# Performance work log

Measured on AMD Instinct MI355X. Metric: run time of the kernel, lower is better.

## Reference

```python
import jax, jax.numpy as jnp
import numpy as np

N = 25000        # nodes
E = 400000       # edges (avg 16 neighbors)
C1 = 8           # output_size (scalar channels into TP)
COUT = 16        # channels_out
LMAX = 2
NB = 8           # number_of_basis
RMAX = 5.0       # max_radius
EMB = 16         # atom embedding dim
NATOM = 10
WNUM = (LMAX + 1) * C1 * COUT                 # per-edge TP weights (parity-shared, k0 paths)
TOTAL_DIM = 2 * COUT * (1 + 3 + 9)            # both parities x ranks 0..2 -> 416


def setup_inputs() -> dict:
    key = jax.random.key(0)
    ks = jax.random.split(key, 12)
    rn = lambda i, shape, s=1.0: jax.random.normal(ks[i], shape, jnp.float32) * s
    pos = rn(0, (N, 3)) * 3.0
    A = jax.random.randint(ks[1], (N,), 0, NATOM)
    batch = jnp.zeros((N,), jnp.int32)                       # single graph
    edge_src = jax.random.randint(ks[2], (E,), 0, N)
    # avoid self-edges (zero-length vectors)
    edge_dst = (edge_src + jax.random.randint(ks[3], (E,), 1, N)) % N
    edge_shifts = jnp.zeros((E, 3), jnp.float32)
    cell = jnp.eye(3, dtype=jnp.float32)[None] * 10.0        # [1,3,3]
    emb_table = rn(4, (NATOM, EMB))
    atom_w1 = rn(5, (EMB, 64), EMB ** -0.5)
    atom_b1 = jnp.zeros((64,), jnp.float32)
    atom_w2 = rn(6, (64, C1), 64 ** -0.5)
    atom_b2 = jnp.zeros((C1,), jnp.float32)
    fc_w1 = rn(7, (NB, 64), NB ** -0.5)
    fc_b1 = jnp.zeros((64,), jnp.float32)
    fc_w2 = rn(8, (64, 64), 64 ** -0.5)
    fc_b2 = jnp.zeros((64,), jnp.float32)
    fc_w3 = rn(9, (64, WNUM), 64 ** -0.5)
    fc_b3 = jnp.zeros((WNUM,), jnp.float32)
    return dict(pos=pos, A=A, batch=batch, edge_src=edge_src, edge_dst=edge_dst,
                edge_shifts=edge_shifts, cell=cell, emb_table=emb_table,
                atom_w1=atom_w1, atom_b1=atom_b1, atom_w2=atom_w2, atom_b2=atom_b2,
                fc_w1=fc_w1, fc_b1=fc_b1, fc_w2=fc_w2, fc_b2=fc_b2, fc_w3=fc_w3, fc_b3=fc_b3)


def reference(pos, A, batch, edge_src, edge_dst, edge_shifts, cell, emb_table,
              atom_w1, atom_b1, atom_w2, atom_b2,
              fc_w1, fc_b1, fc_w2, fc_b2, fc_w3, fc_b3):
    num_edges = edge_src.shape[0]
    num_nodes = pos.shape[0]
    # edge geometry (PBC shift)
    edge_cells = cell[batch[edge_src]]                                   # [E,3,3]
    shift_vecs = jnp.einsum('ni,nij->nj', edge_shifts, edge_cells)
    edge_vec = pos[edge_dst] - pos[edge_src] + shift_vecs                # [E,3]
    edge_length = jnp.sqrt(jnp.sum(edge_vec * edge_vec, axis=1) + 1e-12)
    # per-node scalar features -> gathered to edges
    Ai = jax.nn.silu(emb_table[A] @ atom_w1 + atom_b1) @ atom_w2 + atom_b2  # [N,C1]
    Ai_e = Ai[edge_src]                                                    # [E,C1]
    # edge_rank_powers (normalized): rank-0 scalar 1, rank-1 u, rank-2 u\otimes u
    u = edge_vec / edge_length[:, None]
    # radial basis: e3nn soft_one_hot_linspace (gaussian, cutoff) * sqrt(NB)
    values = jnp.linspace(0.0, RMAX, NB + 2)[1:-1]
    step = RMAX / (NB + 1)
    diff = (edge_length[:, None] - values) / step
    emb = (jnp.exp(-diff * diff) / 1.12) * (NB ** 0.5)                     # [E,NB]
    # radial MLP -> per-edge TP weights
    h = jax.nn.silu(emb @ fc_w1 + fc_b1)
    h = jax.nn.silu(h @ fc_w2 + fc_b2)
    w = (h @ fc_w3 + fc_b3).reshape(num_edges, LMAX + 1, C1, COUT)
    # sparse cartesian O(3) tensor product (k0 paths; only (0,0)x(0,L)->(0,L) nonzero
    # since all x1 L>=1 and parity-1 blocks are zero by construction)
    b0 = jnp.einsum('eco,ec->eo', w[:, 0], Ai_e)                           # [E,COUT]
    b1 = jnp.einsum('eco,ec,ei->eoi', w[:, 1], Ai_e, u)                    # [E,COUT,3]
    b2 = jnp.einsum('eco,ec,ei,ej->eoij', w[:, 2], Ai_e, u, u)             # [E,COUT,3,3]
    feats = jnp.concatenate([b0, b1.reshape(num_edges, -1), b2.reshape(num_edges, -1)], axis=1)
    edge_features = jnp.concatenate([feats, jnp.zeros_like(feats)], axis=1)  # pseudo blocks = 0
    # scatter-sum to destination nodes, normalize by global avg num neighbors
    out = jax.ops.segment_sum(edge_features, edge_dst, num_segments=num_nodes)
    avg_num_neighbors = jnp.maximum(jnp.float32(num_edges) / jnp.float32(num_nodes), 1e-8)
    return out / avg_num_neighbors
```

## Files before the change

### kernel.cpp

```cpp
#include <hip/hip_runtime.h>
#include <math.h>

#define NN 25000
#define NE 400000
#define TD 416
#define TCAP 46080
#define NROWS (TCAP * 10)
#define PLH 64
#define NCAP 64
#define GROWS 32
#define BPT (TCAP / 64)
#define GPB 4

typedef __attribute__((ext_vector_type(8))) __bf16 bf16x8;
typedef __attribute__((ext_vector_type(4))) _Float16 f16x4;
typedef __attribute__((ext_vector_type(4))) float f32x4;

__device__ __forceinline__ float silu_f(float x) {
    return x * __builtin_amdgcn_rcpf(1.0f + __expf(-x));
}

__global__ __launch_bounds__(256) void prep_count_k(
    const float* __restrict__ emb_table,
    const float* __restrict__ aw1, const float* __restrict__ ab1,
    const float* __restrict__ aw2, const float* __restrict__ ab2,
    const float* __restrict__ fw1, const float* __restrict__ fb1,
    const float* __restrict__ fw2,
    const float* __restrict__ fw3, const float* __restrict__ fb3,
    __bf16* __restrict__ w1a, __bf16* __restrict__ w2a,
    __bf16* __restrict__ w3ta, float* __restrict__ b3t,
    const int* __restrict__ esrc, const int* __restrict__ edst,
    const int* __restrict__ A,
    const float* __restrict__ pos, const float* __restrict__ shifts,
    const float* __restrict__ cell, const int* __restrict__ batch,
    int* __restrict__ cnt_dst, int* __restrict__ cnt_t,
    int4* __restrict__ tlist4) {
    const int tid = threadIdx.x;
    if (blockIdx.x < 64) {
        __shared__ float s_ai[80];
        if (tid < 10) {
            float acc[8];
#pragma unroll
            for (int o = 0; o < 8; ++o) acc[o] = ab2[o];
            for (int j = 0; j < 64; ++j) {
                float h = ab1[j];
#pragma unroll
                for (int i = 0; i < 16; ++i) h += emb_table[tid * 16 + i] * aw1[i * 64 + j];
                h = silu_f(h);
#pragma unroll
                for (int o = 0; o < 8; ++o) acc[o] += h * aw2[j * 8 + o];
            }
#pragma unroll
            for (int o = 0; o < 8; ++o) s_ai[tid * 8 + o] = acc[o];
        }
        __syncthreads();
        for (int i = blockIdx.x * 256 + tid; i < 37344; i += 64 * 256) {
            if (i < 2048) {
                int m = i >> 9, r = i & 511, lane = r >> 3, j = r & 7;
                int k = (lane >> 4) * 8 + j, ch = m * 16 + (lane & 15);
                float v = (k < 8) ? fw1[k * 64 + ch] : ((k == 8) ? fb1[ch] : 0.0f);
                w1a[i] = (__bf16)v;
            } else if (i < 6144) {
                int q = i - 2048;
                int mk = q >> 9, lane = (q >> 3) & 63, j = q & 7;
                int m = mk >> 1, kt = mk & 1;
                int k = kt * 32 + (lane >> 4) * 8 + j, ch = m * 16 + (lane & 15);
                w2a[q] = (__bf16)fw2[k * 64 + ch];
            } else if (i < 36864) {
                int q = i - 6144;
                int tmk = q >> 9, lane = (q >> 3) & 63, j = q & 7;
                int kt = tmk & 1, tm = tmk >> 1;
                int t = tm / 3, m = tm - t * 3;
                int k = kt * 32 + (lane >> 4) * 8 + j, ch = m * 16 + (lane & 15);
                int l = ch >> 4, o = ch & 15;
                float s = 0.f;
#pragma unroll
                for (int c = 0; c < 8; ++c)
                    s += s_ai[t * 8 + c] * fw3[k * 384 + l * 128 + c * 16 + o];
                w3ta[q] = (__bf16)s;
            } else {
                int q2 = i - 36864;
                int t = q2 / 48, ch = q2 - t * 48;
                int l = ch >> 4, o = ch & 15;
                float s = 0.f;
#pragma unroll
                for (int c = 0; c < 8; ++c)
                    s += s_ai[t * 8 + c] * fb3[l * 128 + c * 16 + o];
                b3t[q2] = s;
            }
        }
    } else {
        __shared__ int lcnt[10];
        __shared__ int gbase[10];
        if (tid < 10) lcnt[tid] = 0;
        __syncthreads();
        int e = (blockIdx.x - 64) * 256 + tid;
        int t = 0, lr = 0;
        int4 rec;
        bool valid = e < NE;
        if (valid) {
            const int dst = edst[e];
            const int src = esrc[e];
            int rank = atomicAdd(&cnt_dst[dst], 1);
            t = A[src];
            lr = atomicAdd(&lcnt[t], 1);
            const int b = batch[src];
            const float* cb = cell + b * 9;
            const float sh0 = shifts[e * 3 + 0], sh1 = shifts[e * 3 + 1], sh2 = shifts[e * 3 + 2];
            float vx = pos[dst * 3 + 0] - pos[src * 3 + 0] + sh0 * cb[0] + sh1 * cb[3] + sh2 * cb[6];
            float vy = pos[dst * 3 + 1] - pos[src * 3 + 1] + sh0 * cb[1] + sh1 * cb[4] + sh2 * cb[7];
            float vz = pos[dst * 3 + 2] - pos[src * 3 + 2] + sh0 * cb[2] + sh1 * cb[5] + sh2 * cb[8];
            rec.x = __float_as_int(vx);
            rec.y = __float_as_int(vy);
            rec.z = __float_as_int(vz);
            rec.w = (dst << 6) | rank;
        }
        __syncthreads();
        if (tid < 10) gbase[tid] = atomicAdd(&cnt_t[tid], lcnt[tid]);
        __syncthreads();
        if (valid) tlist4[t * TCAP + gbase[t] + lr] = rec;
    }
}

__global__ __launch_bounds__(256) void edge_k(
    const int4* __restrict__ tlist4, const int* __restrict__ cnt_t,
    const __bf16* __restrict__ w1a, const __bf16* __restrict__ w2a,
    const __bf16* __restrict__ w3ta,
    const float* __restrict__ fb2, const float* __restrict__ b3t,
    _Float16* __restrict__ payload) {
    __shared__ __bf16 embuf[GPB][64 * 8];
    __shared__ __bf16 h1buf[GPB][16 * 72];
    __shared__ __bf16 h2buf[GPB][16 * 72];
    __shared__ int pbuf[GPB][64];
    const int tid = threadIdx.x;
    const int wid = tid >> 6, lane = tid & 63;
    const int g = blockIdx.x * GPB + wid;
    const int t_blk = g / BPT;
    const int local = (g - t_blk * BPT) * 64;
    const int nval = cnt_t[t_blk];

    const int idx = min(min(local, nval - 1) + lane, nval - 1);
    const int4 rec = tlist4[t_blk * TCAP + idx];
    const float vx = __int_as_float(rec.x);
    const float vy = __int_as_float(rec.y);
    const float vz = __int_as_float(rec.z);
    const int pd = rec.w;
    pbuf[wid][lane] = pd;

    const float l2 = vx * vx + vy * vy + vz * vz + 1e-12f;
    const float il = __builtin_amdgcn_rsqf(l2);
    const float len = l2 * il;
    {
        const uint4 z4 = {0u, 0u, 0u, 0u};
        union { float f[4]; uint4 u; } uu;
        uu.f[0] = vx * il; uu.f[1] = vy * il; uu.f[2] = vz * il; uu.f[3] = 0.f;
        *(uint4*)(payload + (size_t)pd * PLH + 48) = uu.u;
        *(uint4*)(payload + (size_t)pd * PLH + 56) = z4;
    }

    bf16x8 er0;
#pragma unroll
    for (int k = 0; k < 8; ++k) {
        float d = (len - (5.0f * (float)(k + 1) / 9.0f)) * 1.8f;
        er0[k] = (__bf16)(__expf(-d * d) * 2.525381361380528f);
    }
    *(bf16x8*)&embuf[wid][lane * 8] = er0;

    bf16x8 a1[4], a2[8], a3[6];
#pragma unroll
    for (int m = 0; m < 4; ++m) a1[m] = *(const bf16x8*)(w1a + (m * 64 + lane) * 8);
#pragma unroll
    for (int i = 0; i < 8; ++i) a2[i] = *(const bf16x8*)(w2a + (i * 64 + lane) * 8);
#pragma unroll
    for (int i = 0; i < 6; ++i)
        a3[i] = *(const bf16x8*)(w3ta + ((size_t)(t_blk * 6 + i) * 64 + lane) * 8);
    const int q = lane >> 4;
    const int qr = q * 4;
    const int q8 = q * 8;
    const int colrow = lane & 15;
    f32x4 bias2[4], bias3[3];
#pragma unroll
    for (int m = 0; m < 4; ++m) bias2[m] = *(const f32x4*)(fb2 + m * 16 + qr);
#pragma unroll
    for (int m = 0; m < 3; ++m) bias3[m] = *(const f32x4*)(b3t + t_blk * 48 + m * 16 + qr);

    bf16x8 bone = {};
    bone[0] = (__bf16)1.0f;
    __syncthreads();

    const float SC = (float)NN / (float)NE;
#pragma unroll 1
    for (int n = 0; n < 4; ++n) {
        const int erow = n * 16 + colrow;
        bf16x8 bd = *(bf16x8*)&embuf[wid][erow * 8];
        bf16x8 b1 = (q == 0) ? bd : bone;
#pragma unroll
        for (int m = 0; m < 4; ++m) {
            f32x4 c = {0.f, 0.f, 0.f, 0.f};
            c = __builtin_amdgcn_mfma_f32_16x16x32_bf16(a1[m], b1, c, 0, 0, 0);
            __bf16 hp[4];
#pragma unroll
            for (int r = 0; r < 4; ++r) hp[r] = (__bf16)silu_f(c[r]);
            *(uint2*)&h1buf[wid][colrow * 72 + m * 16 + qr] = *(uint2*)hp;
        }
        __syncthreads();
        bf16x8 b20 = *(bf16x8*)&h1buf[wid][colrow * 72 + q8];
        bf16x8 b21 = *(bf16x8*)&h1buf[wid][colrow * 72 + 32 + q8];
#pragma unroll
        for (int m = 0; m < 4; ++m) {
            f32x4 c = bias2[m];
            c = __builtin_amdgcn_mfma_f32_16x16x32_bf16(a2[m * 2 + 0], b20, c, 0, 0, 0);
            c = __builtin_amdgcn_mfma_f32_16x16x32_bf16(a2[m * 2 + 1], b21, c, 0, 0, 0);
            __bf16 hp[4];
#pragma unroll
            for (int r = 0; r < 4; ++r) hp[r] = (__bf16)silu_f(c[r]);
            *(uint2*)&h2buf[wid][colrow * 72 + m * 16 + qr] = *(uint2*)hp;
        }
        __syncthreads();
        const int prow = pbuf[wid][erow];
        bf16x8 b30 = *(bf16x8*)&h2buf[wid][colrow * 72 + q8];
        bf16x8 b31 = *(bf16x8*)&h2buf[wid][colrow * 72 + 32 + q8];
#pragma unroll
        for (int m = 0; m < 3; ++m) {
            f32x4 c = bias3[m];
            c = __builtin_amdgcn_mfma_f32_16x16x32_bf16(a3[m * 2 + 0], b30, c, 0, 0, 0);
            c = __builtin_amdgcn_mfma_f32_16x16x32_bf16(a3[m * 2 + 1], b31, c, 0, 0, 0);
            f16x4 hp;
#pragma unroll
            for (int r = 0; r < 4; ++r) hp[r] = (_Float16)(c[r] * SC);
            *(f16x4*)(payload + (size_t)prow * PLH + m * 16 + qr) = hp;
        }
    }
}

__global__ __launch_bounds__(256) void gather_k(const int* __restrict__ cnt_dst,
                                                const _Float16* __restrict__ payload,
                                                float* __restrict__ out) {
    __shared__ __align__(16) _Float16 sp_s[GROWS][72];
    __shared__ float sfac[GROWS][16];
    const int n = blockIdx.x;
    const int tid = threadIdx.x;
    const int lo = n * NCAP;
    const int cnt = cnt_dst[n];
    int voff = 0, foff = 0;
    if (tid < 16) { voff = tid; foff = 0; }
    else if (tid < 64) { int q = tid - 16; voff = 16 + q / 3; foff = 1 + q % 3; }
    else if (tid < 208) { int q = tid - 64; voff = 32 + q / 9; foff = 4 + q % 9; }
    float acc = 0.f;
    for (int p0 = 0; p0 < cnt; p0 += GROWS) {
        const int m = min(GROWS, cnt - p0);
        if (tid < m * 8) {
            int r = tid >> 3, q = tid & 7;
            ((uint4*)&sp_s[r][0])[q] = ((const uint4*)(payload + (size_t)(lo + p0 + r) * PLH))[q];
        }
        __syncthreads();
        for (int idx = tid; idx < m * 16; idx += 256) {
            int r = idx >> 4, f = idx & 15;
            if (f < 13) {
                const float* uf = (const float*)&sp_s[r][48];
                float v;
                if (f == 0) v = 1.0f;
                else if (f < 4) v = uf[f - 1];
                else { int g = f - 4; v = uf[g / 3] * uf[g % 3]; }
                sfac[r][f] = v;
            }
        }
        __syncthreads();
        if (tid < 208)
            for (int r = 0; r < m; ++r)
                acc += (float)sp_s[r][voff] * sfac[r][foff];
        __syncthreads();
    }
    if (tid < 208) {
        out[(size_t)n * TD + tid] = acc;
        out[(size_t)n * TD + 208 + tid] = 0.f;
    }
}

extern "C" void kernel_launch(void* const* d_in, const int* in_sizes, int n_in,
                              void* d_out, int out_size, void* d_ws, size_t ws_size,
                              hipStream_t stream) {
    const float* pos       = (const float*)d_in[0];
    const int*   A         = (const int*)d_in[1];
    const int*   batch     = (const int*)d_in[2];
    const int*   esrc      = (const int*)d_in[3];
    const int*   edst      = (const int*)d_in[4];
    const float* shifts    = (const float*)d_in[5];
    const float* cell      = (const float*)d_in[6];
    const float* emb_table = (const float*)d_in[7];
    const float* aw1       = (const float*)d_in[8];
    const float* ab1       = (const float*)d_in[9];
    const float* aw2       = (const float*)d_in[10];
    const float* ab2       = (const float*)d_in[11];
    const float* fw1       = (const float*)d_in[12];
    const float* fb1       = (const float*)d_in[13];
    const float* fw2       = (const float*)d_in[14];
    const float* fb2       = (const float*)d_in[15];
    const float* fw3       = (const float*)d_in[16];
    const float* fb3       = (const float*)d_in[17];
    float* out = (float*)d_out;

    char* base = (char*)d_ws;
    __bf16* w1a    = (__bf16*)(base + 0);
    __bf16* w2a    = (__bf16*)(base + 4096);
    __bf16* w3ta   = (__bf16*)(base + 12288);
    float*  b3t    = (float*)(base + 73728);
    int* cnt_dst   = (int*)(base + 75648);
    int* cnt_t     = (int*)(base + 175680);
    int4* tlist4   = (int4*)(base + 175808);
    _Float16* payload = (_Float16*)(base + 7548672);

    hipMemsetAsync(cnt_dst, 0, 100160, stream);
    prep_count_k<<<64 + (NE + 255) / 256, 256, 0, stream>>>(
        emb_table, aw1, ab1, aw2, ab2, fw1, fb1, fw2, fw3, fb3,
        w1a, w2a, w3ta, b3t, esrc, edst, A, pos, shifts, cell, batch,
        cnt_dst, cnt_t, tlist4);
    edge_k<<<10 * BPT / GPB, 256, 0, stream>>>(tlist4, cnt_t, w1a, w2a, w3ta, fb2, b3t, payload);
    gather_k<<<NN, 256, 0, stream>>>(cnt_dst, payload, out);
}
```

Before: 184.0 us.

## Map one 64-edge group per block with 16 edges per wave

Edge work is redistributed so each block handles one 64-edge group, and each wave processes 16 edges in a single MFMA pass instead of looping four times over 64 edges. Blocks past the valid count exit early, which skips padded groups. Block-wide syncthreads become wave barriers, and the emb and pd shared buffers are removed because each lane now holds its own edge's data. The trade-off is that every wave loads the full set of weight fragments for only 16 edges, raising weight-load traffic per edge, and the grid is four times larger.

```diff
diff --git a/kernel.cpp b/kernel.cpp
--- a/kernel.cpp
+++ b/kernel.cpp
@@ -10,7 +10,6 @@
 #define NCAP 64
 #define GROWS 32
 #define BPT (TCAP / 64)
-#define GPB 4
 
 typedef __attribute__((ext_vector_type(8))) __bf16 bf16x8;
 typedef __attribute__((ext_vector_type(4))) _Float16 f16x4;
@@ -128,29 +127,31 @@
     const __bf16* __restrict__ w3ta,
     const float* __restrict__ fb2, const float* __restrict__ b3t,
     _Float16* __restrict__ payload) {
-    __shared__ __bf16 embuf[GPB][64 * 8];
-    __shared__ __bf16 h1buf[GPB][16 * 72];
-    __shared__ __bf16 h2buf[GPB][16 * 72];
-    __shared__ int pbuf[GPB][64];
+    __shared__ __bf16 h1buf[4][16 * 72];
+    __shared__ __bf16 h2buf[4][16 * 72];
     const int tid = threadIdx.x;
     const int wid = tid >> 6, lane = tid & 63;
-    const int g = blockIdx.x * GPB + wid;
+    const int g = blockIdx.x;
     const int t_blk = g / BPT;
     const int local = (g - t_blk * BPT) * 64;
     const int nval = cnt_t[t_blk];
-
-    const int idx = min(min(local, nval - 1) + lane, nval - 1);
-    const int4 rec = tlist4[t_blk * TCAP + idx];
+    if (local >= nval) return;
+
+    const int colrow = lane & 15;
+    const int q = lane >> 4;
+    const int qr = q * 4, q8 = q * 8;
+
+    const int eidx = min(local + wid * 16 + colrow, nval - 1);
+    const int4 rec = tlist4[t_blk * TCAP + eidx];
     const float vx = __int_as_float(rec.x);
     const float vy = __int_as_float(rec.y);
     const float vz = __int_as_float(rec.z);
     const int pd = rec.w;
-    pbuf[wid][lane] = pd;
 
     const float l2 = vx * vx + vy * vy + vz * vz + 1e-12f;
     const float il = __builtin_amdgcn_rsqf(l2);
     const float len = l2 * il;
-    {
+    if (q == 0) {
         const uint4 z4 = {0u, 0u, 0u, 0u};
         union { float f[4]; uint4 u; } uu;
         uu.f[0] = vx * il; uu.f[1] = vy * il; uu.f[2] = vz * il; uu.f[3] = 0.f;
@@ -164,7 +165,9 @@
         float d = (len - (5.0f * (float)(k + 1) / 9.0f)) * 1.8f;
         er0[k] = (__bf16)(__expf(-d * d) * 2.525381361380528f);
     }
-    *(bf16x8*)&embuf[wid][lane * 8] = er0;
+    bf16x8 bone = {};
+    bone[0] = (__bf16)1.0f;
+    const bf16x8 b1 = (q == 0) ? er0 : bone;
 
     bf16x8 a1[4], a2[8], a3[6];
 #pragma unroll
@@ -174,36 +177,25 @@
 #pragma unroll
     for (int i = 0; i < 6; ++i)
         a3[i] = *(const bf16x8*)(w3ta + ((size_t)(t_blk * 6 + i) * 64 + lane) * 8);
-    const int q = lane >> 4;
-    const int qr = q * 4;
-    const int q8 = q * 8;
-    const int colrow = lane & 15;
     f32x4 bias2[4], bias3[3];
 #pragma unroll
     for (int m = 0; m < 4; ++m) bias2[m] = *(const f32x4*)(fb2 + m * 16 + qr);
 #pragma unroll
     for (int m = 0; m < 3; ++m) bias3[m] = *(const f32x4*)(b3t + t_blk * 48 + m * 16 + qr);
 
-    bf16x8 bone = {};
-    bone[0] = (__bf16)1.0f;
-    __syncthreads();
-
     const float SC = (float)NN / (float)NE;
-#pragma unroll 1
-    for (int n = 0; n < 4; ++n) {
-        const int erow = n * 16 + colrow;
-        bf16x8 bd = *(bf16x8*)&embuf[wid][erow * 8];
-        bf16x8 b1 = (q == 0) ? bd : bone;
-#pragma unroll
-        for (int m = 0; m < 4; ++m) {
-            f32x4 c = {0.f, 0.f, 0.f, 0.f};
-            c = __builtin_amdgcn_mfma_f32_16x16x32_bf16(a1[m], b1, c, 0, 0, 0);
-            __bf16 hp[4];
-#pragma unroll
-            for (int r = 0; r < 4; ++r) hp[r] = (__bf16)silu_f(c[r]);
-            *(uint2*)&h1buf[wid][colrow * 72 + m * 16 + qr] = *(uint2*)hp;
-        }
-        __syncthreads();
+
+#pragma unroll
+    for (int m = 0; m < 4; ++m) {
+        f32x4 c = {0.f, 0.f, 0.f, 0.f};
+        c = __builtin_amdgcn_mfma_f32_16x16x32_bf16(a1[m], b1, c, 0, 0, 0);
+        __bf16 hp[4];
+#pragma unroll
+        for (int r = 0; r < 4; ++r) hp[r] = (__bf16)silu_f(c[r]);
+        *(uint2*)&h1buf[wid][colrow * 72 + m * 16 + qr] = *(uint2*)hp;
+    }
+    __builtin_amdgcn_wave_barrier();
+    {
         bf16x8 b20 = *(bf16x8*)&h1buf[wid][colrow * 72 + q8];
         bf16x8 b21 = *(bf16x8*)&h1buf[wid][colrow * 72 + 32 + q8];
 #pragma unroll
@@ -216,8 +208,9 @@
             for (int r = 0; r < 4; ++r) hp[r] = (__bf16)silu_f(c[r]);
             *(uint2*)&h2buf[wid][colrow * 72 + m * 16 + qr] = *(uint2*)hp;
         }
-        __syncthreads();
-        const int prow = pbuf[wid][erow];
+    }
+    __builtin_amdgcn_wave_barrier();
+    {
         bf16x8 b30 = *(bf16x8*)&h2buf[wid][colrow * 72 + q8];
         bf16x8 b31 = *(bf16x8*)&h2buf[wid][colrow * 72 + 32 + q8];
 #pragma unroll
@@ -228,7 +221,7 @@
             f16x4 hp;
 #pragma unroll
             for (int r = 0; r < 4; ++r) hp[r] = (_Float16)(c[r] * SC);
-            *(f16x4*)(payload + (size_t)prow * PLH + m * 16 + qr) = hp;
+            *(f16x4*)(payload + (size_t)pd * PLH + m * 16 + qr) = hp;
         }
     }
 }
@@ -315,6 +308,6 @@
         emb_table, aw1, ab1, aw2, ab2, fw1, fb1, fw2, fw3, fb3,
         w1a, w2a, w3ta, b3t, esrc, edst, A, pos, shifts, cell, batch,
         cnt_dst, cnt_t, tlist4);
-    edge_k<<<10 * BPT / GPB, 256, 0, stream>>>(tlist4, cnt_t, w1a, w2a, w3ta, fb2, b3t, payload);
+    edge_k<<<10 * BPT, 256, 0, stream>>>(tlist4, cnt_t, w1a, w2a, w3ta, fb2, b3t, payload);
     gather_k<<<NN, 256, 0, stream>>>(cnt_dst, payload, out);
 }
```

After: 189.8 us. 3.2% more time.
